# Kernel tuning notes

Hardware: AMD Instinct MI355X
Metric: run time of the kernel (lower is better)

## Reference

```python
import math
import jax, jax.numpy as jnp
import numpy as np

N, E = 100000, 1600000
F_IN, HID, CLS, H = 128, 64, 40, 2  # per-head channels C = HID = 64, concat width = H*HID = 128


def _lin_params(key, fan_in, fan_out):
    kw, kb = jax.random.split(key)
    s = 1.0 / math.sqrt(fan_in)
    W = jax.random.uniform(kw, (fan_in, fan_out), minval=-s, maxval=s, dtype=jnp.float32)
    b = jax.random.uniform(kb, (fan_out,), minval=-s, maxval=s, dtype=jnp.float32)
    return W, b


def setup_inputs() -> dict:
    key = jax.random.key(0)
    ks = jax.random.split(key, 12)
    x = jax.random.normal(ks[0], (N, F_IN), dtype=jnp.float32)
    edge_index = jax.random.randint(ks[1], (2, E), 0, N, dtype=jnp.int64)
    inp = {"x": x, "edge_index": edge_index}
    # layer 1: in=F_IN(128) -> H*HID(128); layer 2: in=H*HID(128) -> H*HID(128)
    names = ["q1", "k1", "v1", "s1", "q2", "k2", "v2", "s2"]
    fans = [(F_IN, H * HID)] * 4 + [(H * HID, H * HID)] * 4
    for i, (nm, (fi, fo)) in enumerate(zip(names, fans)):
        W, b = _lin_params(ks[2 + i], fi, fo)
        inp["W" + nm] = W
        inp["b" + nm] = b
    Wlin, blin = _lin_params(ks[10], H * HID, CLS)
    inp["Wlin"], inp["blin"] = Wlin, blin
    return inp


def _tconv(x, src, dst, Wq, bq, Wk, bk, Wv, bv, Ws, bs):
    # PyG TransformerConv (concat=True, beta=False, edge_dim=None, root_weight=True)
    n = x.shape[0]
    q = (x @ Wq + bq).reshape(n, H, HID)
    k = (x @ Wk + bk).reshape(n, H, HID)
    v = (x @ Wv + bv).reshape(n, H, HID)
    # per-edge attention score: q_i (dst) dot k_j (src), per head
    alpha = jnp.einsum("ehc,ehc->eh", q[dst], k[src]) / math.sqrt(HID)  # [E, H]
    # segment softmax over incoming edges of each dst node
    m = jax.ops.segment_max(alpha, dst, num_segments=n)
    a = jnp.exp(alpha - m[dst])
    denom = jax.ops.segment_sum(a, dst, num_segments=n)
    a = a / (denom[dst] + 1e-16)
    # weighted scatter-aggregate of values
    msg = v[src] * a[:, :, None]  # [E, H, HID]
    out = jax.ops.segment_sum(msg, dst, num_segments=n).reshape(n, H * HID)
    return out + x @ Ws + bs  # root/skip connection


def reference(x, edge_index, Wq1, bq1, Wk1, bk1, Wv1, bv1, Ws1, bs1,
              Wq2, bq2, Wk2, bk2, Wv2, bv2, Ws2, bs2, Wlin, blin):
    src, dst = edge_index[0], edge_index[1]
    h = _tconv(x, src, dst, Wq1, bq1, Wk1, bk1, Wv1, bv1, Ws1, bs1)
    h = jax.nn.elu(h)  # dropout is identity in eval mode
    h = _tconv(h, src, dst, Wq2, bq2, Wk2, bk2, Wv2, bv2, Ws2, bs2)
    return h @ Wlin + blin  # [N, CLS]
```

## Files before the change

### kernel.cpp

```cpp
#include <hip/hip_runtime.h>
#include <math.h>

#define NNODES 100000
#define NEDGES 1600000
#define FD 128
#define NCLS 40
#define NB_SCAN ((NNODES + 1023) / 1024)

typedef __attribute__((ext_vector_type(8))) short short8v;
typedef __attribute__((ext_vector_type(4))) float f32x4;

__device__ __forceinline__ unsigned short f32_to_bf16_rne(float f) {
    unsigned int u = __float_as_uint(f);
    unsigned int r = u + 0x7fff + ((u >> 16) & 1);
    return (unsigned short)(r >> 16);
}
__device__ __forceinline__ float bf16_to_f32(unsigned short h) {
    return __uint_as_float(((unsigned int)h) << 16);
}


__global__ void detect_kernel(const long long* __restrict__ ei, int* __restrict__ flag_is32) {
    int t = blockIdx.x * blockDim.x + threadIdx.x;
    size_t idx = (size_t)t * (NEDGES / 4096);
    long long v = ei[idx];
    if (v < 0 || v >= NNODES) atomicOr(flag_is32, 1);
}

__device__ __forceinline__ void load_edge(const void* eiv, int is32, int e, int& s, int& d) {
    if (is32) {
        const int* p = (const int*)eiv;
        s = p[e]; d = p[NEDGES + e];
    } else {
        const long long* p = (const long long*)eiv;
        s = (int)p[e]; d = (int)p[NEDGES + e];
    }
}


__global__ void hist_kernel(const void* __restrict__ eiv, const int* __restrict__ flag_is32,
                            int* __restrict__ row_ptr) {
    int is32 = *flag_is32;
    int e = blockIdx.x * blockDim.x + threadIdx.x;
    if (e < NEDGES) {
        int s, d;
        load_edge(eiv, is32, e, s, d);
        atomicAdd(&row_ptr[d + 1], 1);
    }
}

__global__ __launch_bounds__(1024) void scan_blk(int* __restrict__ row_ptr,
                                                 int* __restrict__ cursor,
                                                 int* __restrict__ blk_tot) {
    __shared__ int wtot[16];
    __shared__ int woff[16];
    int t = threadIdx.x, lane = t & 63, wid = t >> 6;
    int i = blockIdx.x * 1024 + t;
    int c = (i < NNODES) ? row_ptr[1 + i] : 0;
    int x = c;
    #pragma unroll
    for (int off = 1; off < 64; off <<= 1) {
        int y = __shfl_up(x, off, 64);
        if (lane >= off) x += y;
    }
    if (lane == 63) wtot[wid] = x;
    __syncthreads();
    if (t < 16) {
        int v = wtot[t];
        #pragma unroll
        for (int off = 1; off < 16; off <<= 1) {
            int y = __shfl_up(v, off, 64);
            if (t >= off) v += y;
        }
        woff[t] = v;
    }
    __syncthreads();
    int excl = (wid == 0) ? 0 : woff[wid - 1];
    int incl = x + excl;
    if (i < NNODES) {
        row_ptr[1 + i] = incl;
        cursor[i]      = incl - c;
    }
    if (t == 0) blk_tot[blockIdx.x] = woff[15];
}

__global__ void scan_tops(const int* __restrict__ blk_tot, int* __restrict__ blk_off) {
    __shared__ int s[128];
    int t = threadIdx.x;
    int c0 = (t < NB_SCAN) ? blk_tot[t] : 0;
    s[t] = c0;
    __syncthreads();
    for (int d = 1; d < 128; d <<= 1) {
        int v = (t >= d) ? s[t - d] : 0;
        __syncthreads();
        s[t] += v;
        __syncthreads();
    }
    if (t < NB_SCAN) blk_off[t] = s[t] - c0;
}

__global__ __launch_bounds__(1024) void scan_add(int* __restrict__ row_ptr,
                                                 int* __restrict__ cursor,
                                                 const int* __restrict__ blk_off) {
    int i = blockIdx.x * 1024 + threadIdx.x;
    if (i < NNODES) {
        int o = blk_off[blockIdx.x];
        row_ptr[1 + i] += o;
        cursor[i]      += o;
    }
}

__global__ void fill_kernel(const void* __restrict__ eiv, const int* __restrict__ flag_is32,
                            int* __restrict__ cursor, int* __restrict__ src_sorted) {
    int is32 = *flag_is32;
    int e = blockIdx.x * blockDim.x + threadIdx.x;
    if (e < NEDGES) {
        int s, d;
        load_edge(eiv, is32, e, s, d);
        int pos = atomicAdd(&cursor[d], 1);
        src_sorted[pos] = s;
    }
}


__global__ void pack_w(const float* __restrict__ W, short* __restrict__ Whi,
                       short* __restrict__ Wlo, int slot) {
    int lane = threadIdx.x;
    int ctkk = blockIdx.x;
    int ct = ctkk >> 2, kk = ctkk & 3;
    int col = ct * 16 + (lane & 15);
    int k0 = kk * 32 + (lane >> 4) * 8;
    short8v h, l;
    #pragma unroll
    for (int j = 0; j < 8; j++) {
        float v = W[(size_t)(k0 + j) * FD + col];
        unsigned short hh = f32_to_bf16_rne(v);
        float rem = v - bf16_to_f32(hh);
        h[j] = (short)hh;
        l[j] = (short)f32_to_bf16_rne(rem);
    }
    size_t o = ((size_t)slot * 32 + ctkk) * 512 + (size_t)lane * 8;
    *(short8v*)(Whi + o) = h;
    *(short8v*)(Wlo + o) = l;
}


__global__ __launch_bounds__(256) void proj_gemm_mfma(
    const float* __restrict__ X,
    const short* __restrict__ Whi, const short* __restrict__ Wlo,
    const float* __restrict__ b0, const float* __restrict__ b1,
    const float* __restrict__ b2, const float* __restrict__ b3,
    float* __restrict__ Q, unsigned short* __restrict__ KV, float* __restrict__ SKIP)
{
    int wid = threadIdx.x >> 6, lane = threadIdx.x & 63;
    int rowbase = blockIdx.x * 64 + wid * 16;
    int r = lane & 15, q = lane >> 4;
    int row = rowbase + r;

    short8v xh[4], xl[4];
    if (row < NNODES) {
        const float* xp = X + (size_t)row * FD + q * 8;
        #pragma unroll
        for (int kk = 0; kk < 4; kk++) {
            float4 v0 = *(const float4*)(xp + kk * 32);
            float4 v1 = *(const float4*)(xp + kk * 32 + 4);
            float vv[8] = {v0.x, v0.y, v0.z, v0.w, v1.x, v1.y, v1.z, v1.w};
            #pragma unroll
            for (int j = 0; j < 8; j++) {
                unsigned short h = f32_to_bf16_rne(vv[j]);
                float rem = vv[j] - bf16_to_f32(h);
                xh[kk][j] = (short)h;
                xl[kk][j] = (short)f32_to_bf16_rne(rem);
            }
        }
    } else {
        short8v z = {0, 0, 0, 0, 0, 0, 0, 0};
        #pragma unroll
        for (int kk = 0; kk < 4; kk++) { xh[kk] = z; xl[kk] = z; }
    }

    #pragma unroll
    for (int pt = 0; pt < 4; pt++) {
        const float* bias = (pt == 0) ? b0 : (pt == 1) ? b1 : (pt == 2) ? b2 : b3;
        #pragma unroll
        for (int ct = 0; ct < 8; ct++) {
            const short* wp = Whi + ((size_t)(pt * 8 + ct) * 4) * 512 + (size_t)lane * 8;
            const short* lp = Wlo + ((size_t)(pt * 8 + ct) * 4) * 512 + (size_t)lane * 8;
            f32x4 acc = {0.f, 0.f, 0.f, 0.f};
            #pragma unroll
            for (int kk = 0; kk < 4; kk++) {
                short8v bh = *(const short8v*)(wp + kk * 512);
                short8v bl = *(const short8v*)(lp + kk * 512);
                acc = __builtin_amdgcn_mfma_f32_16x16x32_bf16(xh[kk], bh, acc, 0, 0, 0);
                acc = __builtin_amdgcn_mfma_f32_16x16x32_bf16(xl[kk], bh, acc, 0, 0, 0);
                acc = __builtin_amdgcn_mfma_f32_16x16x32_bf16(xh[kk], bl, acc, 0, 0, 0);
            }
            float bb = bias[ct * 16 + r];
            int e = ct * 16 + r;
            #pragma unroll
            for (int j = 0; j < 4; j++) {
                int ro = rowbase + q * 4 + j;
                if (ro < NNODES) {
                    float val = acc[j] + bb;
                    if (pt == 0)      Q[(size_t)ro * FD + e] = val;
                    else if (pt == 1) KV[(size_t)ro * 256 + 2 * e]     = f32_to_bf16_rne(val);
                    else if (pt == 2) KV[(size_t)ro * 256 + 2 * e + 1] = f32_to_bf16_rne(val);
                    else              SKIP[(size_t)ro * FD + e] = val;
                }
            }
        }
    }
}


__global__ __launch_bounds__(256) void agg_kernel(
    const float* __restrict__ Q, const unsigned short* __restrict__ KV,
    const float* __restrict__ SKIP, float* __restrict__ OUT,
    const int* __restrict__ row_ptr, const int* __restrict__ src_sorted, int apply_elu)
{
    int wid  = threadIdx.x >> 6;
    int lane = threadIdx.x & 63;
    int half = lane >> 5;
    int sub  = lane & 31;
    int node = blockIdx.x * 4 + wid;
    if (node >= NNODES) return;
    size_t rb = (size_t)node * FD;

    float4 q4 = *(const float4*)(Q + rb + sub * 4);
    q4.x *= 0.125f; q4.y *= 0.125f; q4.z *= 0.125f; q4.w *= 0.125f;

    float s = 0.f;
    float4 acc = make_float4(0.f, 0.f, 0.f, 0.f);
    int e0 = row_ptr[node], e1 = row_ptr[node + 1];
    const uint4* KV4 = (const uint4*)KV;

#define PAIR_UPD(EID)                                                          \
    {                                                                          \
        int eid = (EID);                                                       \
        int valid = eid < e1;                                                  \
        int j = src_sorted[valid ? eid : e1 - 1];                              \
        uint4 wv = KV4[(size_t)j * 32 + sub];                                  \
        float kx = __uint_as_float(wv.x << 16);                                \
        float vx = __uint_as_float(wv.x & 0xffff0000u);                        \
        float ky = __uint_as_float(wv.y << 16);                                \
        float vy = __uint_as_float(wv.y & 0xffff0000u);                        \
        float kz = __uint_as_float(wv.z << 16);                                \
        float vz = __uint_as_float(wv.z & 0xffff0000u);                        \
        float kw = __uint_as_float(wv.w << 16);                                \
        float vw = __uint_as_float(wv.w & 0xffff0000u);                        \
        float p = q4.x * kx + q4.y * ky + q4.z * kz + q4.w * kw;               \
        p += __shfl_xor(p, 1, 64);                                             \
        p += __shfl_xor(p, 2, 64);                                             \
        p += __shfl_xor(p, 4, 64);                                             \
        p += __shfl_xor(p, 8, 64);           \
        float w = valid ? __expf(p) : 0.f;                                     \
        s += w;                                                                \
        acc.x += w * vx; acc.y += w * vy;                                      \
        acc.z += w * vz; acc.w += w * vw;                                      \
    }

    for (int base = e0; base < e1; base += 4) {
        PAIR_UPD(base + half)
        PAIR_UPD(base + 2 + half)
    }
#undef PAIR_UPD

    s += __shfl_xor(s, 32, 64);
    acc.x += __shfl_xor(acc.x, 32, 64);
    acc.y += __shfl_xor(acc.y, 32, 64);
    acc.z += __shfl_xor(acc.z, 32, 64);
    acc.w += __shfl_xor(acc.w, 32, 64);

    if (half == 0) {
        float r = 1.f / (s + 1e-16f);
        float4 sk = *(const float4*)(SKIP + rb + sub * 4);
        float ox = acc.x * r + sk.x;
        float oy = acc.y * r + sk.y;
        float oz = acc.z * r + sk.z;
        float ow = acc.w * r + sk.w;
        if (apply_elu) {
            ox = (ox > 0.f) ? ox : (__expf(ox) - 1.f);
            oy = (oy > 0.f) ? oy : (__expf(oy) - 1.f);
            oz = (oz > 0.f) ? oz : (__expf(oz) - 1.f);
            ow = (ow > 0.f) ? ow : (__expf(ow) - 1.f);
        }
        *(float4*)(OUT + rb + sub * 4) = make_float4(ox, oy, oz, ow);
    }
}


__global__ void final_lin(const float* __restrict__ H, const float* __restrict__ Wl,
                          const float* __restrict__ bl, float* __restrict__ out)
{
    __shared__ float ws[FD * NCLS];
    __shared__ float xs[8][FD + 1];
    int tx = threadIdx.x;
    int ty = threadIdx.y;
    int t = ty * NCLS + tx;
    for (int i = t; i < FD * NCLS; i += 320) ws[i] = Wl[i];
    int row = blockIdx.x * 8;
    for (int i = t; i < 8 * FD; i += 320) {
        int r = i >> 7, c = i & 127;
        xs[r][c] = (row + r < NNODES) ? H[(size_t)(row + r) * FD + c] : 0.f;
    }
    __syncthreads();
    float acc = bl[tx];
    #pragma unroll
    for (int k = 0; k < FD; k++) acc += xs[ty][k] * ws[k * NCLS + tx];
    if (row + ty < NNODES) out[(size_t)(row + ty) * NCLS + tx] = acc;
}


extern "C" void kernel_launch(void* const* d_in, const int* in_sizes, int n_in,
                              void* d_out, int out_size, void* d_ws, size_t ws_size,
                              hipStream_t stream) {
    const float* x  = (const float*)d_in[0];
    const void*  ei = d_in[1];
    const float* Wq1 = (const float*)d_in[2],  *bq1 = (const float*)d_in[3];
    const float* Wk1 = (const float*)d_in[4],  *bk1 = (const float*)d_in[5];
    const float* Wv1 = (const float*)d_in[6],  *bv1 = (const float*)d_in[7];
    const float* Ws1 = (const float*)d_in[8],  *bs1 = (const float*)d_in[9];
    const float* Wq2 = (const float*)d_in[10], *bq2 = (const float*)d_in[11];
    const float* Wk2 = (const float*)d_in[12], *bk2 = (const float*)d_in[13];
    const float* Wv2 = (const float*)d_in[14], *bv2 = (const float*)d_in[15];
    const float* Ws2 = (const float*)d_in[16], *bs2 = (const float*)d_in[17];
    const float* Wlin = (const float*)d_in[18], *blin = (const float*)d_in[19];
    float* out = (float*)d_out;

    const size_t BUFE = (size_t)NNODES * FD;
    float* Qb = (float*)d_ws;
    float* Cb = Qb + BUFE;
    float* Sb = Cb + BUFE;
    unsigned short* KVb = (unsigned short*)(Sb + BUFE);
    int* row_ptr    = (int*)(KVb + (size_t)NNODES * 256);
    int* cursor     = row_ptr + (NNODES + 1);
    int* src_sorted = cursor + NNODES;
    int* flag_is32  = src_sorted + NEDGES;
    int* blk_tot    = flag_is32 + 1;
    int* blk_off    = blk_tot + NB_SCAN;
    uintptr_t pal = ((uintptr_t)(blk_off + NB_SCAN) + 15) & ~(uintptr_t)15;
    short* Whi = (short*)pal;
    short* Wlo = Whi + 8 * 16384;

    const float* Ws[8] = {Wq1, Wk1, Wv1, Ws1, Wq2, Wk2, Wv2, Ws2};
    for (int s = 0; s < 8; s++)
        pack_w<<<32, 64, 0, stream>>>(Ws[s], Whi, Wlo, s);

    hipMemsetAsync(row_ptr, 0, (NNODES + 1) * sizeof(int), stream);
    hipMemsetAsync(flag_is32, 0, sizeof(int), stream);
    detect_kernel<<<16, 256, 0, stream>>>((const long long*)ei, flag_is32);
    hist_kernel<<<(NEDGES + 255) / 256, 256, 0, stream>>>(ei, flag_is32, row_ptr);
    scan_blk<<<NB_SCAN, 1024, 0, stream>>>(row_ptr, cursor, blk_tot);
    scan_tops<<<1, 128, 0, stream>>>(blk_tot, blk_off);
    scan_add<<<NB_SCAN, 1024, 0, stream>>>(row_ptr, cursor, blk_off);
    fill_kernel<<<(NEDGES + 255) / 256, 256, 0, stream>>>(ei, flag_is32, cursor, src_sorted);

    int pgrid = (NNODES + 63) / 64;

    proj_gemm_mfma<<<pgrid, 256, 0, stream>>>(x, Whi, Wlo,
        bq1, bk1, bv1, bs1, Qb, KVb, Sb);
    agg_kernel<<<(NNODES + 3) / 4, 256, 0, stream>>>(Qb, KVb, Sb, Qb,
        row_ptr, src_sorted, 1);

    proj_gemm_mfma<<<pgrid, 256, 0, stream>>>(Qb, Whi + 4 * 16384, Wlo + 4 * 16384,
        bq2, bk2, bv2, bs2, Cb, KVb, Sb);
    agg_kernel<<<(NNODES + 3) / 4, 256, 0, stream>>>(Cb, KVb, Sb, Cb,
        row_ptr, src_sorted, 0);

    final_lin<<<(NNODES + 7) / 8, dim3(NCLS, 8), 0, stream>>>(Cb, Wlin, blin, out);
}
```

Measured before the change: 906.7 us.

## Merge weight packing, fold dtype detection into blocks, co-launch fill with projection

Replaces the eight per-weight pack launches with a single pack_all kernel. Drops the separate detect kernel, memset and global flag; each block now samples the edge index itself and decides int32 vs int64 with a wave ballot. Merges the CSR fill pass into the layer-1 projection GEMM as extra blocks of one launch, so the two independent workloads can overlap and launch count drops. The cost is redundant per-block detection loads and a heterogeneous kernel whose register and LDS needs are set by the GEMM path.

Measured after the change: 804.6 us. 11.3% less time.

```diff
diff --git a/kernel.cpp b/kernel.cpp
--- a/kernel.cpp
+++ b/kernel.cpp
@@ -6,6 +6,8 @@
 #define FD 128
 #define NCLS 40
 #define NB_SCAN ((NNODES + 1023) / 1024)
+#define PGRID ((NNODES + 63) / 64)
+#define FGRID ((NEDGES + 255) / 256)
 
 typedef __attribute__((ext_vector_type(8))) short short8v;
 typedef __attribute__((ext_vector_type(4))) float f32x4;
@@ -20,11 +22,15 @@
 }
 
 
-__global__ void detect_kernel(const long long* __restrict__ ei, int* __restrict__ flag_is32) {
-    int t = blockIdx.x * blockDim.x + threadIdx.x;
-    size_t idx = (size_t)t * (NEDGES / 4096);
-    long long v = ei[idx];
-    if (v < 0 || v >= NNODES) atomicOr(flag_is32, 1);
+__device__ __forceinline__ int detect_is32_block(const void* eiv, int* s_flag) {
+    if (threadIdx.x < 64) {
+        const long long* p = (const long long*)eiv;
+        long long v = p[(size_t)threadIdx.x * (NEDGES / 64)];
+        unsigned long long bad = __ballot(v < 0 || v >= (long long)NNODES);
+        if (threadIdx.x == 0) *s_flag = (bad != 0ULL);
+    }
+    __syncthreads();
+    return *s_flag;
 }
 
 __device__ __forceinline__ void load_edge(const void* eiv, int is32, int e, int& s, int& d) {
@@ -38,9 +44,10 @@
 }
 
 
-__global__ void hist_kernel(const void* __restrict__ eiv, const int* __restrict__ flag_is32,
-                            int* __restrict__ row_ptr) {
-    int is32 = *flag_is32;
+__global__ __launch_bounds__(256) void hist_kernel(const void* __restrict__ eiv,
+                                                   int* __restrict__ row_ptr) {
+    __shared__ int sflag;
+    int is32 = detect_is32_block(eiv, &sflag);
     int e = blockIdx.x * blockDim.x + threadIdx.x;
     if (e < NEDGES) {
         int s, d;
@@ -110,23 +117,20 @@
     }
 }
 
-__global__ void fill_kernel(const void* __restrict__ eiv, const int* __restrict__ flag_is32,
-                            int* __restrict__ cursor, int* __restrict__ src_sorted) {
-    int is32 = *flag_is32;
-    int e = blockIdx.x * blockDim.x + threadIdx.x;
-    if (e < NEDGES) {
-        int s, d;
-        load_edge(eiv, is32, e, s, d);
-        int pos = atomicAdd(&cursor[d], 1);
-        src_sorted[pos] = s;
-    }
-}
-
-
-__global__ void pack_w(const float* __restrict__ W, short* __restrict__ Whi,
-                       short* __restrict__ Wlo, int slot) {
+
+__global__ void pack_all(
+    const float* __restrict__ W0, const float* __restrict__ W1,
+    const float* __restrict__ W2, const float* __restrict__ W3,
+    const float* __restrict__ W4, const float* __restrict__ W5,
+    const float* __restrict__ W6, const float* __restrict__ W7,
+    short* __restrict__ Whi, short* __restrict__ Wlo)
+{
+    int slot = blockIdx.x >> 5;
+    int ctkk = blockIdx.x & 31;
+    const float* W = (slot == 0) ? W0 : (slot == 1) ? W1 : (slot == 2) ? W2 :
+                     (slot == 3) ? W3 : (slot == 4) ? W4 : (slot == 5) ? W5 :
+                     (slot == 6) ? W6 : W7;
     int lane = threadIdx.x;
-    int ctkk = blockIdx.x;
     int ct = ctkk >> 2, kk = ctkk & 3;
     int col = ct * 16 + (lane & 15);
     int k0 = kk * 32 + (lane >> 4) * 8;
@@ -145,7 +149,8 @@
 }
 
 
-__global__ __launch_bounds__(256) void proj_gemm_mfma(
+__device__ __forceinline__ void proj_body(
+    int bx,
     const float* __restrict__ X,
     const short* __restrict__ Whi, const short* __restrict__ Wlo,
     const float* __restrict__ b0, const float* __restrict__ b1,
@@ -153,7 +158,7 @@
     float* __restrict__ Q, unsigned short* __restrict__ KV, float* __restrict__ SKIP)
 {
     int wid = threadIdx.x >> 6, lane = threadIdx.x & 63;
-    int rowbase = blockIdx.x * 64 + wid * 16;
+    int rowbase = bx * 64 + wid * 16;
     int r = lane & 15, q = lane >> 4;
     int row = rowbase + r;
 
@@ -212,6 +217,40 @@
     }
 }
 
+__global__ __launch_bounds__(256) void proj_gemm_mfma(
+    const float* __restrict__ X,
+    const short* __restrict__ Whi, const short* __restrict__ Wlo,
+    const float* __restrict__ b0, const float* __restrict__ b1,
+    const float* __restrict__ b2, const float* __restrict__ b3,
+    float* __restrict__ Q, unsigned short* __restrict__ KV, float* __restrict__ SKIP)
+{
+    proj_body(blockIdx.x, X, Whi, Wlo, b0, b1, b2, b3, Q, KV, SKIP);
+}
+
+
+__global__ __launch_bounds__(256) void proj1_fill(
+    const float* __restrict__ X,
+    const short* __restrict__ Whi, const short* __restrict__ Wlo,
+    const float* __restrict__ b0, const float* __restrict__ b1,
+    const float* __restrict__ b2, const float* __restrict__ b3,
+    float* __restrict__ Q, unsigned short* __restrict__ KV, float* __restrict__ SKIP,
+    const void* __restrict__ eiv, int* __restrict__ cursor, int* __restrict__ src_sorted)
+{
+    if (blockIdx.x < PGRID) {
+        proj_body(blockIdx.x, X, Whi, Wlo, b0, b1, b2, b3, Q, KV, SKIP);
+    } else {
+        __shared__ int sflag;
+        int is32 = detect_is32_block(eiv, &sflag);
+        int e = (blockIdx.x - PGRID) * 256 + threadIdx.x;
+        if (e < NEDGES) {
+            int s, d;
+            load_edge(eiv, is32, e, s, d);
+            int pos = atomicAdd(&cursor[d], 1);
+            src_sorted[pos] = s;
+        }
+    }
+}
+
 
 __global__ __launch_bounds__(256) void agg_kernel(
     const float* __restrict__ Q, const unsigned short* __restrict__ KV,
@@ -335,34 +374,25 @@
     int* row_ptr    = (int*)(KVb + (size_t)NNODES * 256);
     int* cursor     = row_ptr + (NNODES + 1);
     int* src_sorted = cursor + NNODES;
-    int* flag_is32  = src_sorted + NEDGES;
-    int* blk_tot    = flag_is32 + 1;
+    int* blk_tot    = src_sorted + NEDGES;
     int* blk_off    = blk_tot + NB_SCAN;
     uintptr_t pal = ((uintptr_t)(blk_off + NB_SCAN) + 15) & ~(uintptr_t)15;
     short* Whi = (short*)pal;
     short* Wlo = Whi + 8 * 16384;
 
-    const float* Ws[8] = {Wq1, Wk1, Wv1, Ws1, Wq2, Wk2, Wv2, Ws2};
-    for (int s = 0; s < 8; s++)
-        pack_w<<<32, 64, 0, stream>>>(Ws[s], Whi, Wlo, s);
-
     hipMemsetAsync(row_ptr, 0, (NNODES + 1) * sizeof(int), stream);
-    hipMemsetAsync(flag_is32, 0, sizeof(int), stream);
-    detect_kernel<<<16, 256, 0, stream>>>((const long long*)ei, flag_is32);
-    hist_kernel<<<(NEDGES + 255) / 256, 256, 0, stream>>>(ei, flag_is32, row_ptr);
+    pack_all<<<256, 64, 0, stream>>>(Wq1, Wk1, Wv1, Ws1, Wq2, Wk2, Wv2, Ws2, Whi, Wlo);
+    hist_kernel<<<FGRID, 256, 0, stream>>>(ei, row_ptr);
     scan_blk<<<NB_SCAN, 1024, 0, stream>>>(row_ptr, cursor, blk_tot);
     scan_tops<<<1, 128, 0, stream>>>(blk_tot, blk_off);
     scan_add<<<NB_SCAN, 1024, 0, stream>>>(row_ptr, cursor, blk_off);
-    fill_kernel<<<(NEDGES + 255) / 256, 256, 0, stream>>>(ei, flag_is32, cursor, src_sorted);
-
-    int pgrid = (NNODES + 63) / 64;
-
-    proj_gemm_mfma<<<pgrid, 256, 0, stream>>>(x, Whi, Wlo,
-        bq1, bk1, bv1, bs1, Qb, KVb, Sb);
+
+    proj1_fill<<<PGRID + FGRID, 256, 0, stream>>>(x, Whi, Wlo,
+        bq1, bk1, bv1, bs1, Qb, KVb, Sb, ei, cursor, src_sorted);
     agg_kernel<<<(NNODES + 3) / 4, 256, 0, stream>>>(Qb, KVb, Sb, Qb,
         row_ptr, src_sorted, 1);
 
-    proj_gemm_mfma<<<pgrid, 256, 0, stream>>>(Qb, Whi + 4 * 16384, Wlo + 4 * 16384,
+    proj_gemm_mfma<<<PGRID, 256, 0, stream>>>(Qb, Whi + 4 * 16384, Wlo + 4 * 16384,
         bq2, bk2, bv2, bs2, Cb, KVb, Sb);
     agg_kernel<<<(NNODES + 3) / 4, 256, 0, stream>>>(Cb, KVb, Sb, Cb,
         row_ptr, src_sorted, 0);
```
